# Performance work log

Measured on AMD Instinct MI355X. Metric: run time of the kernel, lower is better.

## Reference

```python
import jax, jax.numpy as jnp
import numpy as np

LEAKY_ALPHA = 0.2  # tf.nn.leaky_relu default

def setup_inputs() -> dict:
    key = jax.random.key(0)
    k1, k2, k3 = jax.random.split(key, 3)
    B, N, F, U = 4, 4096, 128, 64
    x = jax.random.normal(k1, (B, N, F), dtype=jnp.float32)
    W = jax.random.normal(k2, (F, U), dtype=jnp.float32) * (1.0 / np.sqrt(F))
    a = jax.random.normal(k3, (2 * U, 1), dtype=jnp.float32) * (1.0 / np.sqrt(2 * U))
    return {"x": x, "W": W, "a": a}

def reference(x, W, a):
    # h: (B, N, U)
    h = jnp.einsum('bnf,fu->bnu', x, W)
    U = h.shape[-1]
    a1 = a[:U, 0]   # attends to source node i
    a2 = a[U:, 0]   # attends to target node j
    # a^T [h_i || h_j] = a1^T h_i + a2^T h_j  (same math, no O(N^2*2U) concat)
    f1 = jnp.einsum('bnu,u->bn', h, a1)  # (B, N)
    f2 = jnp.einsum('bnu,u->bn', h, a2)  # (B, N)
    e = f1[:, :, None] + f2[:, None, :]  # (B, N, N)
    e = jnp.where(e >= 0, e, LEAKY_ALPHA * e)
    attn = jax.nn.softmax(e, axis=-1)    # softmax over j
    return jnp.einsum('bij,bju->biu', attn, h)
```

## Files before the change

### kernel.cpp

```cpp
#include <hip/hip_runtime.h>
#include <hip/hip_bf16.h>

#define NBATCH 4
#define NN 4096
#define NF 128
#define NU 64
#define CHUNK 64
#define NCHUNK (NN / CHUNK)
#define LEAKY 0.2f

__global__ __launch_bounds__(256) void k1_h(
    const float* __restrict__ x, const float* __restrict__ W,
    const float* __restrict__ a,
    float* __restrict__ h, float* __restrict__ f1, float* __restrict__ f2) {
  __shared__ float Ws[NF][NU];
  __shared__ float xs[64][NF];
  __shared__ float a1s[NU], a2s[NU];
  int tid = threadIdx.x;
  for (int k = tid; k < NF * NU; k += 256) ((float*)Ws)[k] = W[k];
  if (tid < NU) { a1s[tid] = a[tid]; a2s[tid] = a[NU + tid]; }
  int row0 = blockIdx.x * 64;
  for (int k = tid; k < 64 * NF; k += 256)
    ((float*)xs)[k] = x[(size_t)row0 * NF + k];
  __syncthreads();
  int u = tid & 63;
  int wv = tid >> 6;
  for (int rr = 0; rr < 16; ++rr) {
    int lr = wv * 16 + rr;
    float acc = 0.f;
#pragma unroll
    for (int f = 0; f < NF; f += 4) {
      float4 xv = *(const float4*)&xs[lr][f];
      acc += xv.x * Ws[f][u] + xv.y * Ws[f + 1][u]
           + xv.z * Ws[f + 2][u] + xv.w * Ws[f + 3][u];
    }
    int grow = row0 + lr;
    h[(size_t)grow * NU + u] = acc;
    float p1 = acc * a1s[u], p2 = acc * a2s[u];
#pragma unroll
    for (int off = 32; off >= 1; off >>= 1) {
      p1 += __shfl_xor(p1, off, 64);
      p2 += __shfl_xor(p2, off, 64);
    }
    if (u == 0) { f1[grow] = p1; f2[grow] = p2; }
  }
}

__global__ __launch_bounds__(256) void k2a_count(
    const float* __restrict__ f2, unsigned short* __restrict__ pc) {
  __shared__ float fsk[256];
  int b = blockIdx.x >> 8;
  int jc = (blockIdx.x >> 4) & 15;
  int kc = blockIdx.x & 15;
  int tid = threadIdx.x;
  const float* f2b = f2 + b * NN;
  fsk[tid] = f2b[kc * 256 + tid];
  __syncthreads();
  int j = jc * 256 + tid;
  float my = f2b[j];
  int lim = j - kc * 256;
  int cnt = 0;
#pragma unroll 8
  for (int k = 0; k < 256; ++k) {
    float v = fsk[k];
    cnt += (v < my) || (v == my && k < lim);
  }
  pc[((size_t)(b * 16 + kc)) * NN + j] = (unsigned short)cnt;
}

__global__ __launch_bounds__(256) void k2b_scatter(
    const float* __restrict__ f2, const unsigned short* __restrict__ pc,
    int* __restrict__ perm, float* __restrict__ f2s,
    float* __restrict__ whi, float* __restrict__ wlo) {
  int b = blockIdx.x >> 4;
  int jc = blockIdx.x & 15;
  int j = jc * 256 + threadIdx.x;
  float my = f2[b * NN + j];
  int rank = 0;
#pragma unroll
  for (int kc = 0; kc < 16; ++kc)
    rank += pc[((size_t)(b * 16 + kc)) * NN + j];
  int o = b * NN + rank;
  perm[o] = j;
  f2s[o] = my;
  whi[o] = expf(my);
  wlo[o] = expf(LEAKY * my);
}

__global__ __launch_bounds__(128) void k3_scan(
    const float* __restrict__ h, const int* __restrict__ perm,
    const float* __restrict__ whi, const float* __restrict__ wlo,
    float* __restrict__ LPhi, float* __restrict__ LPlo,
    float* __restrict__ LPshi, float* __restrict__ LPslo,
    float* __restrict__ CThi, float* __restrict__ CTlo,
    float* __restrict__ CTshi, float* __restrict__ CTslo) {
  __shared__ int pj[CHUNK];
  __shared__ float wh[CHUNK], wl[CHUNK];
  int b = blockIdx.x >> 6;
  int chunk = blockIdx.x & 63;
  int k0 = b * NN + chunk * CHUNK;
  int tid = threadIdx.x;
  if (tid < CHUNK) {
    pj[tid] = perm[k0 + tid];
    wh[tid] = whi[k0 + tid];
    wl[tid] = wlo[k0 + tid];
  }
  __syncthreads();
  int u = tid & 63;
  bool hi = tid < 64;
  float* LP = hi ? LPhi : LPlo;
  float* LPs = hi ? LPshi : LPslo;
  const float* hb = h + (size_t)b * NN * NU;
  float acc = 0.f, sacc = 0.f;
  for (int k = 0; k < CHUNK; ++k) {
    float w = hi ? wh[k] : wl[k];
    int j = pj[k];
    acc += w * hb[(size_t)j * NU + u];
    LP[(size_t)(k0 + k) * NU + u] = acc;
    if (u == 0) { sacc += w; LPs[k0 + k] = sacc; }
  }
  float* CT = hi ? CThi : CTlo;
  CT[(size_t)(b * (NCHUNK + 1) + chunk) * NU + u] = acc;
  if (u == 0) (hi ? CTshi : CTslo)[b * (NCHUNK + 1) + chunk] = sacc;
}

__global__ __launch_bounds__(256) void k3b_ct(
    float* __restrict__ CThi, float* __restrict__ CTlo,
    float* __restrict__ CTshi, float* __restrict__ CTslo) {
  int wid = blockIdx.x * 4 + (threadIdx.x >> 6);
  int lane = threadIdx.x & 63;
  if (wid < 512) {
    int b = wid >> 7;
    int half = (wid >> 6) & 1;
    int u = wid & 63;
    float* CT = (half == 0) ? CThi : CTlo;
    size_t idx = (size_t)(b * (NCHUNK + 1) + lane) * NU + u;
    float v = CT[idx];
#pragma unroll
    for (int off = 1; off < 64; off <<= 1) {
      float t = __shfl_up(v, off, 64);
      if (lane >= off) v += t;
    }
    float excl = __shfl_up(v, 1, 64);
    if (lane == 0) excl = 0.f;
    CT[idx] = excl;
    if (lane == 63) CT[(size_t)(b * (NCHUNK + 1) + NCHUNK) * NU + u] = v;
  } else if (wid < 520) {
    int s = wid - 512;
    int b = s >> 1;
    float* CTs = ((s & 1) == 0) ? CTshi : CTslo;
    float v = CTs[b * (NCHUNK + 1) + lane];
#pragma unroll
    for (int off = 1; off < 64; off <<= 1) {
      float t = __shfl_up(v, off, 64);
      if (lane >= off) v += t;
    }
    float excl = __shfl_up(v, 1, 64);
    if (lane == 0) excl = 0.f;
    CTs[b * (NCHUNK + 1) + lane] = excl;
    if (lane == 63) CTs[b * (NCHUNK + 1) + NCHUNK] = v;
  }
}

__global__ __launch_bounds__(256) void k4_out(
    const float* __restrict__ f1, const float* __restrict__ f2s,
    const float* __restrict__ LPhi, const float* __restrict__ LPlo,
    const float* __restrict__ LPshi, const float* __restrict__ LPslo,
    const float* __restrict__ CThi, const float* __restrict__ CTlo,
    const float* __restrict__ CTshi, const float* __restrict__ CTslo,
    float* __restrict__ out) {
  int tid = threadIdx.x;
  int u = tid & 63;
  int wv = tid >> 6;
  int row = blockIdx.x * 4 + wv;
  int b = row >> 12;
  const float* fs = f2s + b * NN;
  float fv = f1[row];
  float theta = -fv;
  int lo = 0, hiN = NN;
#pragma unroll
  for (int it = 0; it < 12; ++it) {
    int mid = (lo + hiN) >> 1;
    if (fs[mid] < theta) lo = mid + 1; else hiN = mid;
  }
  int t = lo;
  float e1 = expf(fv), e1l = expf(LEAKY * fv);
  float Phi = 0.f, Plo = 0.f, Pshi = 0.f, Pslo = 0.f;
  if (t > 0) {
    int c = (t - 1) >> 6;
    size_t ctidx = (size_t)(b * (NCHUNK + 1) + c) * NU + u;
    size_t lpidx = ((size_t)b * NN + (t - 1)) * NU + u;
    Phi = CThi[ctidx] + LPhi[lpidx];
    Plo = CTlo[ctidx] + LPlo[lpidx];
    Pshi = CTshi[b * (NCHUNK + 1) + c] + LPshi[b * NN + t - 1];
    Pslo = CTslo[b * (NCHUNK + 1) + c] + LPslo[b * NN + t - 1];
  }
  float Thi = CThi[(size_t)(b * (NCHUNK + 1) + NCHUNK) * NU + u];
  float Dtot = CTshi[b * (NCHUNK + 1) + NCHUNK];
  float Ahi = Thi - Phi;
  float Alo = Plo;
  float den = e1 * (Dtot - Pshi) + e1l * Pslo;
  float num = e1 * Ahi + e1l * Alo;
  out[(size_t)row * NU + u] = num / den;
}

extern "C" void kernel_launch(void* const* d_in, const int* in_sizes, int n_in,
                              void* d_out, int out_size, void* d_ws, size_t ws_size,
                              hipStream_t stream) {
  const float* x = (const float*)d_in[0];
  const float* W = (const float*)d_in[1];
  const float* a = (const float*)d_in[2];
  float* out = (float*)d_out;
  float* ws = (float*)d_ws;

  size_t o = 0;
  float* h    = ws + o; o += (size_t)NBATCH * NN * NU;
  float* f1   = ws + o; o += (size_t)NBATCH * NN;
  float* f2   = ws + o; o += (size_t)NBATCH * NN;
  int*  perm  = (int*)(ws + o); o += (size_t)NBATCH * NN;
  float* f2s  = ws + o; o += (size_t)NBATCH * NN;
  float* whi  = ws + o; o += (size_t)NBATCH * NN;
  float* wlo  = ws + o; o += (size_t)NBATCH * NN;
  float* LPhi = ws + o; o += (size_t)NBATCH * NN * NU;
  float* LPlo = ws + o; o += (size_t)NBATCH * NN * NU;
  float* LPshi= ws + o; o += (size_t)NBATCH * NN;
  float* LPslo= ws + o; o += (size_t)NBATCH * NN;
  float* CThi = ws + o; o += (size_t)NBATCH * (NCHUNK + 1) * NU;
  float* CTlo = ws + o; o += (size_t)NBATCH * (NCHUNK + 1) * NU;
  float* CTshi= ws + o; o += (size_t)NBATCH * (NCHUNK + 1);
  float* CTslo= ws + o; o += (size_t)NBATCH * (NCHUNK + 1);
  unsigned short* pc = (unsigned short*)(ws + o); o += (size_t)NBATCH * 16 * NN / 2;

  k1_h<<<(NBATCH * NN) / 64, 256, 0, stream>>>(x, W, a, h, f1, f2);
  k2a_count<<<NBATCH * 256, 256, 0, stream>>>(f2, pc);
  k2b_scatter<<<NBATCH * 16, 256, 0, stream>>>(f2, pc, perm, f2s, whi, wlo);
  k3_scan<<<NBATCH * NCHUNK, 128, 0, stream>>>(h, perm, whi, wlo,
      LPhi, LPlo, LPshi, LPslo, CThi, CTlo, CTshi, CTslo);
  k3b_ct<<<130, 256, 0, stream>>>(CThi, CTlo, CTshi, CTslo);
  k4_out<<<(NBATCH * NN) / 4, 256, 0, stream>>>(f1, f2s,
      LPhi, LPlo, LPshi, LPslo, CThi, CTlo, CTshi, CTslo, out);
}
```

Before: 130.6 us.

## Replace per-element prefix arrays with chunk sums and in-chunk recompute

The scan stage no longer writes full per-element prefix arrays (two N×U float buffers per batch). It now computes only per-chunk totals over chunks of 32, scans those across chunks, and has the output kernel recompute the partial chunk straddling the threshold directly from h, perm and the weights. The 12-step binary search is replaced by a two-level wavefront ballot/popcount search. The projection kernel also drops the staging of W into shared memory, reads W from global memory directly and accumulates 8 rows per thread. The goal is to cut the large workspace writes and reads, at the cost of 32 gathered h rows per output row in the final kernel.

```diff
diff --git a/kernel.cpp b/kernel.cpp
--- a/kernel.cpp
+++ b/kernel.cpp
@@ -5,38 +5,40 @@
 #define NN 4096
 #define NF 128
 #define NU 64
-#define CHUNK 64
-#define NCHUNK (NN / CHUNK)
+#define CH 32
+#define NCH (NN / CH)
 #define LEAKY 0.2f
 
 __global__ __launch_bounds__(256) void k1_h(
     const float* __restrict__ x, const float* __restrict__ W,
     const float* __restrict__ a,
     float* __restrict__ h, float* __restrict__ f1, float* __restrict__ f2) {
-  __shared__ float Ws[NF][NU];
-  __shared__ float xs[64][NF];
-  __shared__ float a1s[NU], a2s[NU];
+  __shared__ float xs[32][NF];
   int tid = threadIdx.x;
-  for (int k = tid; k < NF * NU; k += 256) ((float*)Ws)[k] = W[k];
-  if (tid < NU) { a1s[tid] = a[tid]; a2s[tid] = a[NU + tid]; }
-  int row0 = blockIdx.x * 64;
-  for (int k = tid; k < 64 * NF; k += 256)
-    ((float*)xs)[k] = x[(size_t)row0 * NF + k];
+  int row0 = blockIdx.x * 32;
+  const float4* xg = (const float4*)(x + (size_t)row0 * NF);
+  float4* xs4 = (float4*)xs;
+  for (int k = tid; k < 32 * NF / 4; k += 256) xs4[k] = xg[k];
   __syncthreads();
   int u = tid & 63;
   int wv = tid >> 6;
-  for (int rr = 0; rr < 16; ++rr) {
-    int lr = wv * 16 + rr;
-    float acc = 0.f;
-#pragma unroll
-    for (int f = 0; f < NF; f += 4) {
-      float4 xv = *(const float4*)&xs[lr][f];
-      acc += xv.x * Ws[f][u] + xv.y * Ws[f + 1][u]
-           + xv.z * Ws[f + 2][u] + xv.w * Ws[f + 3][u];
-    }
-    int grow = row0 + lr;
-    h[(size_t)grow * NU + u] = acc;
-    float p1 = acc * a1s[u], p2 = acc * a2s[u];
+  float acc[8] = {0.f,0.f,0.f,0.f,0.f,0.f,0.f,0.f};
+#pragma unroll 4
+  for (int f = 0; f < NF; f += 4) {
+    float w0 = W[(f+0)*NU+u], w1 = W[(f+1)*NU+u],
+          w2 = W[(f+2)*NU+u], w3 = W[(f+3)*NU+u];
+#pragma unroll
+    for (int r = 0; r < 8; ++r) {
+      float4 xv = *(const float4*)&xs[wv*8+r][f];
+      acc[r] += xv.x*w0 + xv.y*w1 + xv.z*w2 + xv.w*w3;
+    }
+  }
+  float a1 = a[u], a2 = a[NU+u];
+#pragma unroll
+  for (int r = 0; r < 8; ++r) {
+    int grow = row0 + wv*8 + r;
+    h[(size_t)grow*NU+u] = acc[r];
+    float p1 = acc[r]*a1, p2 = acc[r]*a2;
 #pragma unroll
     for (int off = 32; off >= 1; off >>= 1) {
       p1 += __shfl_xor(p1, off, 64);
@@ -87,121 +89,121 @@
   wlo[o] = expf(LEAKY * my);
 }
 
-__global__ __launch_bounds__(128) void k3_scan(
+__global__ __launch_bounds__(256) void k3_csum(
     const float* __restrict__ h, const int* __restrict__ perm,
     const float* __restrict__ whi, const float* __restrict__ wlo,
-    float* __restrict__ LPhi, float* __restrict__ LPlo,
-    float* __restrict__ LPshi, float* __restrict__ LPslo,
-    float* __restrict__ CThi, float* __restrict__ CTlo,
-    float* __restrict__ CTshi, float* __restrict__ CTslo) {
-  __shared__ int pj[CHUNK];
-  __shared__ float wh[CHUNK], wl[CHUNK];
-  int b = blockIdx.x >> 6;
-  int chunk = blockIdx.x & 63;
-  int k0 = b * NN + chunk * CHUNK;
-  int tid = threadIdx.x;
-  if (tid < CHUNK) {
-    pj[tid] = perm[k0 + tid];
-    wh[tid] = whi[k0 + tid];
-    wl[tid] = wlo[k0 + tid];
-  }
-  __syncthreads();
-  int u = tid & 63;
-  bool hi = tid < 64;
-  float* LP = hi ? LPhi : LPlo;
-  float* LPs = hi ? LPshi : LPslo;
+    float* __restrict__ Pvhi, float* __restrict__ Pvlo,
+    float* __restrict__ Pshi, float* __restrict__ Pslo) {
+  int u = threadIdx.x & 63;
+  int wv = threadIdx.x >> 6;
+  int cg = blockIdx.x * 4 + wv;
+  int b = cg >> 7;
+  int c = cg & (NCH - 1);
+  int k0 = b * NN + c * CH;
   const float* hb = h + (size_t)b * NN * NU;
-  float acc = 0.f, sacc = 0.f;
-  for (int k = 0; k < CHUNK; ++k) {
-    float w = hi ? wh[k] : wl[k];
-    int j = pj[k];
-    acc += w * hb[(size_t)j * NU + u];
-    LP[(size_t)(k0 + k) * NU + u] = acc;
-    if (u == 0) { sacc += w; LPs[k0 + k] = sacc; }
-  }
-  float* CT = hi ? CThi : CTlo;
-  CT[(size_t)(b * (NCHUNK + 1) + chunk) * NU + u] = acc;
-  if (u == 0) (hi ? CTshi : CTslo)[b * (NCHUNK + 1) + chunk] = sacc;
-}
-
-__global__ __launch_bounds__(256) void k3b_ct(
-    float* __restrict__ CThi, float* __restrict__ CTlo,
-    float* __restrict__ CTshi, float* __restrict__ CTslo) {
+  float ah = 0.f, al = 0.f, sh = 0.f, sl = 0.f;
+#pragma unroll
+  for (int k = 0; k < CH; ++k) {
+    int j = perm[k0 + k];
+    float wh = whi[k0 + k], wl = wlo[k0 + k];
+    float hv = hb[(size_t)j * NU + u];
+    ah += wh * hv; al += wl * hv; sh += wh; sl += wl;
+  }
+  size_t o = (size_t)(b * (NCH + 1) + c) * NU + u;
+  Pvhi[o] = ah; Pvlo[o] = al;
+  if (u == 0) { Pshi[b * (NCH + 1) + c] = sh; Pslo[b * (NCH + 1) + c] = sl; }
+}
+
+__global__ __launch_bounds__(256) void k3b_scan(
+    float* __restrict__ Pvhi, float* __restrict__ Pvlo,
+    float* __restrict__ Pshi, float* __restrict__ Pslo) {
   int wid = blockIdx.x * 4 + (threadIdx.x >> 6);
-  int lane = threadIdx.x & 63;
+  int l = threadIdx.x & 63;
   if (wid < 512) {
     int b = wid >> 7;
     int half = (wid >> 6) & 1;
     int u = wid & 63;
-    float* CT = (half == 0) ? CThi : CTlo;
-    size_t idx = (size_t)(b * (NCHUNK + 1) + lane) * NU + u;
-    float v = CT[idx];
+    float* T = half ? Pvlo : Pvhi;
+    size_t i0 = (size_t)(b * (NCH + 1) + 2 * l) * NU + u;
+    size_t i1 = (size_t)(b * (NCH + 1) + 2 * l + 1) * NU + u;
+    float v0 = T[i0], v1 = T[i1];
+    float pair = v0 + v1, s = pair;
 #pragma unroll
     for (int off = 1; off < 64; off <<= 1) {
-      float t = __shfl_up(v, off, 64);
-      if (lane >= off) v += t;
-    }
-    float excl = __shfl_up(v, 1, 64);
-    if (lane == 0) excl = 0.f;
-    CT[idx] = excl;
-    if (lane == 63) CT[(size_t)(b * (NCHUNK + 1) + NCHUNK) * NU + u] = v;
+      float t = __shfl_up(s, off, 64);
+      if (l >= off) s += t;
+    }
+    float excl = s - pair;
+    T[i0] = excl;
+    T[i1] = excl + v0;
+    if (l == 63) T[(size_t)(b * (NCH + 1) + NCH) * NU + u] = s;
   } else if (wid < 520) {
-    int s = wid - 512;
-    int b = s >> 1;
-    float* CTs = ((s & 1) == 0) ? CTshi : CTslo;
-    float v = CTs[b * (NCHUNK + 1) + lane];
+    int s2 = wid - 512;
+    int b = s2 >> 1;
+    float* T = (s2 & 1) ? Pslo : Pshi;
+    float v0 = T[b * (NCH + 1) + 2 * l], v1 = T[b * (NCH + 1) + 2 * l + 1];
+    float pair = v0 + v1, s = pair;
 #pragma unroll
     for (int off = 1; off < 64; off <<= 1) {
-      float t = __shfl_up(v, off, 64);
-      if (lane >= off) v += t;
-    }
-    float excl = __shfl_up(v, 1, 64);
-    if (lane == 0) excl = 0.f;
-    CTs[b * (NCHUNK + 1) + lane] = excl;
-    if (lane == 63) CTs[b * (NCHUNK + 1) + NCHUNK] = v;
+      float t = __shfl_up(s, off, 64);
+      if (l >= off) s += t;
+    }
+    float excl = s - pair;
+    T[b * (NCH + 1) + 2 * l] = excl;
+    T[b * (NCH + 1) + 2 * l + 1] = excl + v0;
+    if (l == 63) T[b * (NCH + 1) + NCH] = s;
   }
 }
 
 __global__ __launch_bounds__(256) void k4_out(
     const float* __restrict__ f1, const float* __restrict__ f2s,
-    const float* __restrict__ LPhi, const float* __restrict__ LPlo,
-    const float* __restrict__ LPshi, const float* __restrict__ LPslo,
-    const float* __restrict__ CThi, const float* __restrict__ CTlo,
-    const float* __restrict__ CTshi, const float* __restrict__ CTslo,
+    const float* __restrict__ h, const int* __restrict__ perm,
+    const float* __restrict__ whi, const float* __restrict__ wlo,
+    const float* __restrict__ Pvhi, const float* __restrict__ Pvlo,
+    const float* __restrict__ Pshi, const float* __restrict__ Pslo,
     float* __restrict__ out) {
-  int tid = threadIdx.x;
-  int u = tid & 63;
-  int wv = tid >> 6;
+  int u = threadIdx.x & 63;
+  int wv = threadIdx.x >> 6;
   int row = blockIdx.x * 4 + wv;
   int b = row >> 12;
   const float* fs = f2s + b * NN;
   float fv = f1[row];
   float theta = -fv;
-  int lo = 0, hiN = NN;
-#pragma unroll
-  for (int it = 0; it < 12; ++it) {
-    int mid = (lo + hiN) >> 1;
-    if (fs[mid] < theta) lo = mid + 1; else hiN = mid;
-  }
-  int t = lo;
+  float q1 = fs[u * 64 + 63];
+  int n1 = __popcll(__ballot(q1 < theta));
+  int t;
+  if (n1 == 64) {
+    t = NN;
+  } else {
+    float q2 = fs[n1 * 64 + u];
+    t = n1 * 64 + __popcll(__ballot(q2 < theta));
+  }
+  int c = t >> 5; if (c > NCH - 1) c = NCH - 1;
+  int k0 = b * NN + c * CH;
+  const float* hb = h + (size_t)b * NN * NU;
+  float ch = 0.f, cl = 0.f, csh = 0.f, csl = 0.f;
+#pragma unroll
+  for (int k = 0; k < CH; ++k) {
+    int kg = c * CH + k;
+    int j = perm[k0 + k];
+    float hv = hb[(size_t)j * NU + u];
+    float wh = whi[k0 + k], wl = wlo[k0 + k];
+    bool hi = (kg >= t);
+    float wH = hi ? wh : 0.f;
+    float wL = hi ? 0.f : wl;
+    ch += wH * hv; cl += wL * hv; csh += wH; csl += wL;
+  }
+  size_t base = (size_t)b * (NCH + 1);
+  size_t oc0 = (base + c) * NU + u;
+  size_t oc1 = (base + c + 1) * NU + u;
+  size_t oT  = (base + NCH) * NU + u;
+  float Ahi = (Pvhi[oT] - Pvhi[oc1]) + ch;
+  float Alo = Pvlo[oc0] + cl;
+  float Shi = (Pshi[base + NCH] - Pshi[base + c + 1]) + csh;
+  float Slo = Pslo[base + c] + csl;
   float e1 = expf(fv), e1l = expf(LEAKY * fv);
-  float Phi = 0.f, Plo = 0.f, Pshi = 0.f, Pslo = 0.f;
-  if (t > 0) {
-    int c = (t - 1) >> 6;
-    size_t ctidx = (size_t)(b * (NCHUNK + 1) + c) * NU + u;
-    size_t lpidx = ((size_t)b * NN + (t - 1)) * NU + u;
-    Phi = CThi[ctidx] + LPhi[lpidx];
-    Plo = CTlo[ctidx] + LPlo[lpidx];
-    Pshi = CTshi[b * (NCHUNK + 1) + c] + LPshi[b * NN + t - 1];
-    Pslo = CTslo[b * (NCHUNK + 1) + c] + LPslo[b * NN + t - 1];
-  }
-  float Thi = CThi[(size_t)(b * (NCHUNK + 1) + NCHUNK) * NU + u];
-  float Dtot = CTshi[b * (NCHUNK + 1) + NCHUNK];
-  float Ahi = Thi - Phi;
-  float Alo = Plo;
-  float den = e1 * (Dtot - Pshi) + e1l * Pslo;
-  float num = e1 * Ahi + e1l * Alo;
-  out[(size_t)row * NU + u] = num / den;
+  float den = e1 * Shi + e1l * Slo;
+  out[(size_t)row * NU + u] = (e1 * Ahi + e1l * Alo) / den;
 }
 
 extern "C" void kernel_launch(void* const* d_in, const int* in_sizes, int n_in,
@@ -221,22 +223,18 @@
   float* f2s  = ws + o; o += (size_t)NBATCH * NN;
   float* whi  = ws + o; o += (size_t)NBATCH * NN;
   float* wlo  = ws + o; o += (size_t)NBATCH * NN;
-  float* LPhi = ws + o; o += (size_t)NBATCH * NN * NU;
-  float* LPlo = ws + o; o += (size_t)NBATCH * NN * NU;
-  float* LPshi= ws + o; o += (size_t)NBATCH * NN;
-  float* LPslo= ws + o; o += (size_t)NBATCH * NN;
-  float* CThi = ws + o; o += (size_t)NBATCH * (NCHUNK + 1) * NU;
-  float* CTlo = ws + o; o += (size_t)NBATCH * (NCHUNK + 1) * NU;
-  float* CTshi= ws + o; o += (size_t)NBATCH * (NCHUNK + 1);
-  float* CTslo= ws + o; o += (size_t)NBATCH * (NCHUNK + 1);
+  float* Pvhi = ws + o; o += (size_t)NBATCH * (NCH + 1) * NU;
+  float* Pvlo = ws + o; o += (size_t)NBATCH * (NCH + 1) * NU;
+  float* Pshi = ws + o; o += (size_t)NBATCH * (NCH + 1);
+  float* Pslo = ws + o; o += (size_t)NBATCH * (NCH + 1);
   unsigned short* pc = (unsigned short*)(ws + o); o += (size_t)NBATCH * 16 * NN / 2;
 
-  k1_h<<<(NBATCH * NN) / 64, 256, 0, stream>>>(x, W, a, h, f1, f2);
+  k1_h<<<(NBATCH * NN) / 32, 256, 0, stream>>>(x, W, a, h, f1, f2);
   k2a_count<<<NBATCH * 256, 256, 0, stream>>>(f2, pc);
   k2b_scatter<<<NBATCH * 16, 256, 0, stream>>>(f2, pc, perm, f2s, whi, wlo);
-  k3_scan<<<NBATCH * NCHUNK, 128, 0, stream>>>(h, perm, whi, wlo,
-      LPhi, LPlo, LPshi, LPslo, CThi, CTlo, CTshi, CTslo);
-  k3b_ct<<<130, 256, 0, stream>>>(CThi, CTlo, CTshi, CTslo);
-  k4_out<<<(NBATCH * NN) / 4, 256, 0, stream>>>(f1, f2s,
-      LPhi, LPlo, LPshi, LPslo, CThi, CTlo, CTshi, CTslo, out);
-}
+  k3_csum<<<(NBATCH * NCH) / 4, 256, 0, stream>>>(h, perm, whi, wlo,
+      Pvhi, Pvlo, Pshi, Pslo);
+  k3b_scan<<<130, 256, 0, stream>>>(Pvhi, Pvlo, Pshi, Pslo);
+  k4_out<<<(NBATCH * NN) / 4, 256, 0, stream>>>(f1, f2s, h, perm, whi, wlo,
+      Pvhi, Pvlo, Pshi, Pslo, out);
+}
```

Result: faster. 116.4 us (-10.8%).
